# Performance work log

Measured on AMD Instinct MI355X. Metric: run time of the kernel, lower is better.

The kernel has to match this reference:

```python
import jax, jax.numpy as jnp
import numpy as np

B, C, H, W = 8, 512, 32, 32
NH = 8
DH = C // NH
HW = H * W
LN_EPS = 1e-5
NORM_EPS = 1e-12  # torch F.normalize eps


def setup_inputs() -> dict:
    key = jax.random.key(0)
    ks = jax.random.split(key, 8)
    s = 0.02
    return {
        "x": jax.random.normal(ks[0], (B, C, H, W), dtype=jnp.float32),
        "qkv_w": jax.random.normal(ks[1], (3 * C, C), dtype=jnp.float32) * s,
        "proj_w": jax.random.normal(ks[2], (C, C), dtype=jnp.float32) * s,
        "proj_b": jnp.zeros((C,), dtype=jnp.float32),
        "temperature": jnp.ones((NH, 1, 1), dtype=jnp.float32),
        "ln_g": jnp.ones((C,), dtype=jnp.float32),
        "ln_b": jnp.zeros((C,), dtype=jnp.float32),
        "pos_embed": jax.random.normal(ks[3], (1, HW, C), dtype=jnp.float32) * s,
        "dw_w": jax.random.normal(ks[4], (C, 1, 3, 3), dtype=jnp.float32) * s,
        "dw_b": jnp.zeros((C,), dtype=jnp.float32),
        "pw_w": jax.random.normal(ks[5], (C, C, 1, 1), dtype=jnp.float32) * s,
        "pw_b": jnp.zeros((C,), dtype=jnp.float32),
    }


def _l2norm_tokens(t):
    # normalize along token axis (dim=-2), like F.normalize(t, dim=-2)
    n = jnp.sqrt(jnp.sum(t * t, axis=-2, keepdims=True))
    return t / jnp.maximum(n, NORM_EPS)


def _layernorm(t, g, b):
    mu = jnp.mean(t, axis=-1, keepdims=True)
    var = jnp.mean((t - mu) ** 2, axis=-1, keepdims=True)
    return (t - mu) * jax.lax.rsqrt(var + LN_EPS) * g + b


def _dsconv(t, dw_w, dw_b, pw_w, pw_b):
    # depthwise 3x3 SAME + pointwise 1x1, NCHW / OIHW
    y = jax.lax.conv_general_dilated(
        t, dw_w, window_strides=(1, 1), padding="SAME",
        dimension_numbers=("NCHW", "OIHW", "NCHW"), feature_group_count=C)
    y = y + dw_b[None, :, None, None]
    y = jax.lax.conv_general_dilated(
        y, pw_w, window_strides=(1, 1), padding="SAME",
        dimension_numbers=("NCHW", "OIHW", "NCHW"))
    return y + pw_b[None, :, None, None]


def reference(x, qkv_w, proj_w, proj_b, temperature, ln_g, ln_b, pos_embed, dw_w, dw_b, pw_w, pw_b):
    save = x
    t = jnp.transpose(x.reshape(B, C, HW), (0, 2, 1))  # [B, HW, C]
    t = t + pos_embed
    # qkv projection (no bias)
    qkv = t @ qkv_w.T  # [B, HW, 3C]
    qkv = qkv.reshape(B, HW, 3, NH, DH).transpose(2, 0, 3, 1, 4)  # [3,B,NH,HW,DH]
    q, k, v = qkv[0], qkv[1], qkv[2]
    q = _l2norm_tokens(q)
    k = _l2norm_tokens(k)
    attn = jnp.einsum("bhnd,bhmd->bhnm", q, k) * temperature[None]  # [B,NH,HW,HW]
    attn = jax.nn.softmax(attn, axis=-1)
    o = jnp.einsum("bhnm,bhmd->bhnd", attn, v)  # [B,NH,HW,DH]
    o = o.transpose(0, 2, 1, 3).reshape(B, HW, C)
    o = o @ proj_w.T + proj_b
    o = _layernorm(o, ln_g, ln_b)
    o = jnp.transpose(o, (0, 2, 1)).reshape(B, C, H, W)
    o = o + save
    return o + _dsconv(o, dw_w, dw_b, pw_w, pw_b)
```

## Files before the change

kernel.cpp:

```cpp
#include <hip/hip_runtime.h>
#include <math.h>

#define BB_ 8
#define C_ 512
#define C3_ 1536
#define HW_ 1024
#define NH_ 8
#define DH_ 64
#define HH_ 32
#define WW_ 32

typedef __attribute__((ext_vector_type(8))) short short8;
typedef __attribute__((ext_vector_type(8))) unsigned short ushort8;
typedef __attribute__((ext_vector_type(4))) unsigned short ushort4_t;
typedef __attribute__((ext_vector_type(4))) float f32x4;
typedef unsigned short ushort;

__device__ inline ushort f2bf(float f) {
  union { float f; unsigned u; } v;
  v.f = f;
  unsigned r = v.u + 0x7fffu + ((v.u >> 16) & 1u);
  return (ushort)(r >> 16);
}
__device__ inline float bf2f(ushort u) {
  union { unsigned u; float f; } v;
  v.u = ((unsigned)u) << 16;
  return v.f;
}

#define GLD16(gptr, lptr)                                                     \
  __builtin_amdgcn_global_load_lds(                                           \
      (const __attribute__((address_space(1))) unsigned int*)(gptr),          \
      (__attribute__((address_space(3))) unsigned int*)(lptr), 16, 0, 0)

__global__ void cvt_weights_kernel(const float* __restrict__ qkv_w,
                                   const float* __restrict__ proj_w,
                                   const float* __restrict__ pw_w,
                                   ushort* __restrict__ dst) {
  int i = blockIdx.x * 256 + threadIdx.x;
  if (i < 786432) dst[i] = f2bf(qkv_w[i]);
  else if (i < 1048576) dst[i] = f2bf(proj_w[i - 786432]);
  else dst[i] = f2bf(pw_w[i - 1048576]);
}

__global__ __launch_bounds__(256) void add_pos_kernel(
    const float* __restrict__ x, const float* __restrict__ pos,
    ushort* __restrict__ t, ushort* __restrict__ xT) {
  __shared__ float tile[64][65];
  const int tid = threadIdx.x;
  const int n0 = blockIdx.x * 64, c0 = blockIdx.y * 64, b = blockIdx.z;
#pragma unroll
  for (int it = 0; it < 4; it++) {
    int c_l = (tid >> 4) + it * 16;
    int n_l4 = (tid & 15) * 4;
    float4 v = *(const float4*)&x[((size_t)(b * C_ + c0 + c_l)) * HW_ + n0 + n_l4];
    tile[c_l][n_l4 + 0] = v.x;
    tile[c_l][n_l4 + 1] = v.y;
    tile[c_l][n_l4 + 2] = v.z;
    tile[c_l][n_l4 + 3] = v.w;
  }
  __syncthreads();
#pragma unroll
  for (int it = 0; it < 4; it++) {
    int n_l = (tid >> 4) + it * 16;
    int c_l4 = (tid & 15) * 4;
    size_t token = (size_t)(b * HW_ + n0 + n_l);
    float4 pv = *(const float4*)&pos[(n0 + n_l) * C_ + c0 + c_l4];
    float xv0 = tile[c_l4 + 0][n_l], xv1 = tile[c_l4 + 1][n_l];
    float xv2 = tile[c_l4 + 2][n_l], xv3 = tile[c_l4 + 3][n_l];
    ushort4_t tb = {f2bf(xv0 + pv.x), f2bf(xv1 + pv.y), f2bf(xv2 + pv.z),
                    f2bf(xv3 + pv.w)};
    ushort4_t xb = {f2bf(xv0), f2bf(xv1), f2bf(xv2), f2bf(xv3)};
    *(ushort4_t*)&t[token * C_ + c0 + c_l4] = tb;
    *(ushort4_t*)&xT[token * C_ + c0 + c_l4] = xb;
  }
}

__global__ __launch_bounds__(256) void gemm_128(
    const ushort* __restrict__ A, const ushort* __restrict__ Wm,
    ushort* __restrict__ out, int N, int K) {
  __shared__ alignas(16) ushort As[128 * 32];
  __shared__ alignas(16) ushort Bs[128 * 32];
  const int bn = blockIdx.x * 128, bm = blockIdx.y * 128;
  const int tid = threadIdx.x;
  const int w = tid >> 6, lane = tid & 63;
  const int wm = 64 * (w & 1), wn = 64 * (w >> 1);
  const int l15 = lane & 15, lq = lane >> 4;

  f32x4 acc[4][4];
#pragma unroll
  for (int i = 0; i < 4; i++)
#pragma unroll
    for (int j = 0; j < 4; j++) acc[i][j] = (f32x4){0.f, 0.f, 0.f, 0.f};

  const int srr = lane >> 2, sq1 = lane & 3;

  for (int k0 = 0; k0 < K; k0 += 32) {
    __syncthreads();
#pragma unroll
    for (int j = 0; j < 2; j++) {
      int r = 32 * w + 16 * j + srr;
      int q = (sq1 - (r >> 1)) & 3;
      GLD16(A + (size_t)(bm + r) * K + k0 + q * 8, &As[(32 * w + 16 * j) * 32]);
      GLD16(Wm + (size_t)(bn + r) * K + k0 + q * 8, &Bs[(32 * w + 16 * j) * 32]);
    }
    __syncthreads();
    short8 af[4], bf[4];
#pragma unroll
    for (int nt = 0; nt < 4; nt++) {
      int r = wm + nt * 16 + l15;
      af[nt] = *(const short8*)&As[r * 32 + (((lq + (r >> 1)) & 3) * 8)];
      int c = wn + nt * 16 + l15;
      bf[nt] = *(const short8*)&Bs[c * 32 + (((lq + (c >> 1)) & 3) * 8)];
    }
#pragma unroll
    for (int i = 0; i < 4; i++)
#pragma unroll
      for (int j = 0; j < 4; j++)
        acc[i][j] = __builtin_amdgcn_mfma_f32_16x16x32_bf16(af[i], bf[j],
                                                            acc[i][j], 0, 0, 0);
  }

#pragma unroll
  for (int i = 0; i < 4; i++) {
#pragma unroll
    for (int j = 0; j < 4; j++) {
      int c = bn + wn + j * 16 + l15;
#pragma unroll
      for (int r = 0; r < 4; r++) {
        int m = bm + wm + i * 16 + lq * 4 + r;
        out[(size_t)m * N + c] = f2bf(acc[i][j][r]);
      }
    }
  }
}

template <int EPI>
__global__ __launch_bounds__(256) void gemm_n64(
    const ushort* __restrict__ A, const ushort* __restrict__ Wm,
    const float* __restrict__ bias, float* __restrict__ out,
    const float* __restrict__ resid, int N, int K) {
  __shared__ alignas(16) ushort As[128 * 32];
  __shared__ alignas(16) ushort Bs[64 * 32];
  const int bn = blockIdx.x * 64, bm = blockIdx.y * 128;
  const int tid = threadIdx.x;
  const int w = tid >> 6, lane = tid & 63;
  const int wm = 64 * (w & 1), wn = 32 * (w >> 1);
  const int l15 = lane & 15, lq = lane >> 4;

  f32x4 acc[4][2];
#pragma unroll
  for (int i = 0; i < 4; i++)
#pragma unroll
    for (int j = 0; j < 2; j++) acc[i][j] = (f32x4){0.f, 0.f, 0.f, 0.f};

  const int srr = lane >> 2, sq1 = lane & 3;

  for (int k0 = 0; k0 < K; k0 += 32) {
    __syncthreads();
#pragma unroll
    for (int j = 0; j < 2; j++) {
      int r = 32 * w + 16 * j + srr;
      int q = (sq1 - (r >> 1)) & 3;
      GLD16(A + (size_t)(bm + r) * K + k0 + q * 8, &As[(32 * w + 16 * j) * 32]);
    }
    {
      int r = 16 * w + srr;
      int q = (sq1 - (r >> 1)) & 3;
      GLD16(Wm + (size_t)(bn + r) * K + k0 + q * 8, &Bs[(16 * w) * 32]);
    }
    __syncthreads();
    short8 af[4], bf[2];
#pragma unroll
    for (int nt = 0; nt < 4; nt++) {
      int r = wm + nt * 16 + l15;
      af[nt] = *(const short8*)&As[r * 32 + (((lq + (r >> 1)) & 3) * 8)];
    }
#pragma unroll
    for (int j = 0; j < 2; j++) {
      int c = wn + j * 16 + l15;
      bf[j] = *(const short8*)&Bs[c * 32 + (((lq + (c >> 1)) & 3) * 8)];
    }
#pragma unroll
    for (int i = 0; i < 4; i++)
#pragma unroll
      for (int j = 0; j < 2; j++)
        acc[i][j] = __builtin_amdgcn_mfma_f32_16x16x32_bf16(af[i], bf[j],
                                                            acc[i][j], 0, 0, 0);
  }

#pragma unroll
  for (int i = 0; i < 4; i++) {
#pragma unroll
    for (int j = 0; j < 2; j++) {
      int c = bn + wn + j * 16 + l15;
      float bv = bias[c];
#pragma unroll
      for (int r = 0; r < 4; r++) {
        int m = bm + wm + i * 16 + lq * 4 + r;
        float v = acc[i][j][r] + bv;
        if (EPI == 1) {
          out[(size_t)m * N + c] = v;
        } else {
          int b = m >> 10, s = m & (HW_ - 1);
          out[((size_t)(b * C_ + c)) * HW_ + s] = v + resid[(size_t)m * C_ + c];
        }
      }
    }
  }
}

__global__ __launch_bounds__(256) void qk_norms_stage1(
    const ushort* __restrict__ qkv, float* __restrict__ partials) {
  __shared__ float smq[32][65], smk[32][65];
  const int blk = blockIdx.x;
  const int bh = blk >> 3, seg = blk & 7;
  const int b = bh >> 3, h = bh & 7;
  const int tid = threadIdx.x;
  const int trow = tid >> 3, chunk = tid & 7;
  float sq[8] = {}, sk[8] = {};
  const ushort* base = qkv + (size_t)b * HW_ * C3_ + h * 64 + chunk * 8;
#pragma unroll
  for (int i = 0; i < 4; i++) {
    int n = seg * 128 + i * 32 + trow;
    const ushort* p = base + (size_t)n * C3_;
    ushort8 q8 = *(const ushort8*)p;
    ushort8 k8 = *(const ushort8*)(p + C_);
#pragma unroll
    for (int j = 0; j < 8; j++) {
      float qv = bf2f(q8[j]), kv = bf2f(k8[j]);
      sq[j] += qv * qv;
      sk[j] += kv * kv;
    }
  }
#pragma unroll
  for (int j = 0; j < 8; j++) {
    smq[trow][chunk * 8 + j] = sq[j];
    smk[trow][chunk * 8 + j] = sk[j];
  }
  __syncthreads();
  if (tid < 64) {
    float s = 0.f;
    for (int i = 0; i < 32; i++) s += smq[i][tid];
    partials[((size_t)(bh * 8 + seg) * 2 + 0) * 64 + tid] = s;
  } else if (tid < 128) {
    int d = tid - 64;
    float s = 0.f;
    for (int i = 0; i < 32; i++) s += smk[i][d];
    partials[((size_t)(bh * 8 + seg) * 2 + 1) * 64 + d] = s;
  }
}

__global__ void qk_norms_stage2(const float* __restrict__ partials,
                                float* __restrict__ invq,
                                float* __restrict__ invk) {
  const int bh = blockIdx.x;
  const int tid = threadIdx.x;
  const int which = tid >> 6, d = tid & 63;
  float s = 0.f;
#pragma unroll
  for (int seg = 0; seg < 8; seg++)
    s += partials[((size_t)(bh * 8 + seg) * 2 + which) * 64 + d];
  float r = 1.0f / fmaxf(sqrtf(s), 1e-12f);
  if (which == 0) invq[bh * 64 + d] = r;
  else invk[bh * 64 + d] = r;
}

__global__ __launch_bounds__(512) void attn_mfma_kernel(
    const ushort* __restrict__ qkv, const float* __restrict__ invq,
    const float* __restrict__ invk, const float* __restrict__ temp,
    ushort* __restrict__ o) {
  __shared__ alignas(16) ushort Ks[64 * 64];
  __shared__ alignas(16) ushort Vts[64][88];
  __shared__ alignas(16) ushort Ps[8][16][88];

  const int tid = threadIdx.x;
  const int w = tid >> 6, lane = tid & 63;
  const int qgrp = lane >> 4, lcol = lane & 15;
  const int bh = blockIdx.x >> 3;
  const int qt = blockIdx.x & 7;
  const int b = bh >> 3, h = bh & 7;
  const int q0 = qt * 128;

  short8 qf[2];
  {
    const int m = q0 + w * 16 + lcol;
    const ushort* qrow = qkv + ((size_t)(b * HW_ + m)) * C3_ + h * 64;
    const float tmp = temp[h];
#pragma unroll
    for (int kc = 0; kc < 2; kc++) {
      union { short8 v; ushort u[8]; } pk;
#pragma unroll
      for (int j = 0; j < 8; j++) {
        int d = kc * 32 + qgrp * 8 + j;
        float s = invq[bh * 64 + d] * invk[bh * 64 + d] * tmp;
        pk.u[j] = f2bf(bf2f(qrow[d]) * s);
      }
      qf[kc] = pk.v;
    }
  }

  f32x4 of[4];
  float lsum[4] = {0.f, 0.f, 0.f, 0.f};
#pragma unroll
  for (int nt = 0; nt < 4; nt++) of[nt] = (f32x4){0.f, 0.f, 0.f, 0.f};

  const ushort* kg = qkv + (size_t)b * HW_ * C3_ + C_ + h * 64;

  const int srow = tid >> 3;
  const int sc = tid & 7;
  const int scg = sc ^ (srow & 7);
  const int vcol = (((srow >> 3) + sc) & 7) * 8 + (srow & 7);

  for (int kt = 0; kt < 16; kt++) {
    __syncthreads();
    GLD16(kg + (size_t)(kt * 64 + srow) * C3_ + scg * 8, &Ks[w * 512]);
    {
      const ushort* vsrc = kg + C_ + (size_t)(kt * 64 + srow) * C3_ + sc * 8;
      ushort8 vv = *(const ushort8*)vsrc;
#pragma unroll
      for (int j = 0; j < 8; j++) Vts[sc * 8 + j][vcol] = vv[j];
    }
    __syncthreads();

    f32x4 sfr[4];
#pragma unroll
    for (int nt = 0; nt < 4; nt++) sfr[nt] = (f32x4){0.f, 0.f, 0.f, 0.f};
#pragma unroll
    for (int kc = 0; kc < 2; kc++) {
#pragma unroll
      for (int nt = 0; nt < 4; nt++) {
        int row = nt * 16 + lcol;
        short8 kf = *(const short8*)
            &Ks[row * 64 + (((kc * 4 + qgrp) ^ (row & 7)) * 8)];
        sfr[nt] =
            __builtin_amdgcn_mfma_f32_16x16x32_bf16(qf[kc], kf, sfr[nt], 0, 0, 0);
      }
    }

#pragma unroll
    for (int nt = 0; nt < 4; nt++) {
#pragma unroll
      for (int r = 0; r < 4; r++) {
        float e = __expf(sfr[nt][r]);
        lsum[r] += e;
        Ps[w][qgrp * 4 + r][nt * 16 + lcol] = f2bf(e);
      }
    }

#pragma unroll
    for (int kc = 0; kc < 2; kc++) {
      short8 pf = *(const short8*)&Ps[w][lcol][kc * 32 + qgrp * 8];
#pragma unroll
      for (int nt = 0; nt < 4; nt++) {
        int d = nt * 16 + lcol;
        int cph = ((kc * 4 + qgrp) + (d >> 3)) & 7;
        short8 vf = *(const short8*)&Vts[d][cph * 8];
        of[nt] =
            __builtin_amdgcn_mfma_f32_16x16x32_bf16(pf, vf, of[nt], 0, 0, 0);
      }
    }
  }

  float inv[4];
#pragma unroll
  for (int r = 0; r < 4; r++) {
    float s = lsum[r];
    s += __shfl_xor(s, 1);
    s += __shfl_xor(s, 2);
    s += __shfl_xor(s, 4);
    s += __shfl_xor(s, 8);
    inv[r] = 1.0f / s;
  }
#pragma unroll
  for (int nt = 0; nt < 4; nt++) {
#pragma unroll
    for (int r = 0; r < 4; r++) {
      int m = q0 + w * 16 + qgrp * 4 + r;
      o[((size_t)(b * HW_ + m)) * C_ + h * 64 + nt * 16 + lcol] =
          f2bf(of[nt][r] * inv[r]);
    }
  }
}

__global__ void ln_residual_kernel(float* __restrict__ po, const ushort* xT,
                                   const float* __restrict__ g,
                                   const float* __restrict__ bb, ushort* ybf) {
  int token = blockIdx.x;
  int t = threadIdx.x;
  float* row = po + (size_t)token * C_;
  float v0 = row[t], v1 = row[t + 256];
  float s = v0 + v1;
#pragma unroll
  for (int off = 32; off; off >>= 1) s += __shfl_xor(s, off);
  __shared__ float wr[4];
  if ((t & 63) == 0) wr[t >> 6] = s;
  __syncthreads();
  float mu = (wr[0] + wr[1] + wr[2] + wr[3]) * (1.0f / C_);
  float d0 = v0 - mu, d1 = v1 - mu;
  float vs = d0 * d0 + d1 * d1;
#pragma unroll
  for (int off = 32; off; off >>= 1) vs += __shfl_xor(vs, off);
  __syncthreads();
  if ((t & 63) == 0) wr[t >> 6] = vs;
  __syncthreads();
  float var = (wr[0] + wr[1] + wr[2] + wr[3]) * (1.0f / C_);
  float rstd = rsqrtf(var + 1e-5f);
  float r0 = bf2f(xT[(size_t)token * C_ + t]);
  float r1 = bf2f(xT[(size_t)token * C_ + t + 256]);
  float o0 = d0 * rstd * g[t] + bb[t] + r0;
  float o1 = d1 * rstd * g[t + 256] + bb[t + 256] + r1;
  row[t] = o0;
  row[t + 256] = o1;
  ybf[(size_t)token * C_ + t] = f2bf(o0);
  ybf[(size_t)token * C_ + t + 256] = f2bf(o1);
}

__global__ __launch_bounds__(256) void dwconv_kernel(
    const ushort* __restrict__ y, const float* __restrict__ w,
    const float* __restrict__ bias, ushort* __restrict__ out) {
  const int cg = threadIdx.x & 63, tg = threadIdx.x >> 6;
  const int c0 = cg * 8;
  float wreg[9][8], breg[8];
#pragma unroll
  for (int j = 0; j < 8; j++) {
    breg[j] = bias[c0 + j];
#pragma unroll
    for (int kk = 0; kk < 9; kk++) wreg[kk][j] = w[(c0 + j) * 9 + kk];
  }
  for (int i = 0; i < 4; i++) {
    int token = blockIdx.x * 16 + tg * 4 + i;
    int b = token >> 10, s = token & (HW_ - 1);
    int hh = s >> 5, ww = s & 31;
    float acc[8];
#pragma unroll
    for (int j = 0; j < 8; j++) acc[j] = breg[j];
#pragma unroll
    for (int ky = 0; ky < 3; ky++) {
      int yy = hh + ky - 1;
      if (yy < 0 || yy >= HH_) continue;
#pragma unroll
      for (int kx = 0; kx < 3; kx++) {
        int xx = ww + kx - 1;
        if (xx < 0 || xx >= WW_) continue;
        ushort8 v8 = *(const ushort8*)
            &y[((size_t)(b * HW_ + yy * 32 + xx)) * C_ + c0];
        const float* wk = wreg[ky * 3 + kx];
#pragma unroll
        for (int j = 0; j < 8; j++) acc[j] += wk[j] * bf2f(v8[j]);
      }
    }
    ushort8 pk;
#pragma unroll
    for (int j = 0; j < 8; j++) pk[j] = f2bf(acc[j]);
    *(ushort8*)&out[(size_t)token * C_ + c0] = pk;
  }
}

extern "C" void kernel_launch(void* const* d_in, const int* in_sizes, int n_in,
                              void* d_out, int out_size, void* d_ws,
                              size_t ws_size, hipStream_t stream) {
  const float* x = (const float*)d_in[0];
  const float* qkv_w = (const float*)d_in[1];
  const float* proj_w = (const float*)d_in[2];
  const float* proj_b = (const float*)d_in[3];
  const float* temperature = (const float*)d_in[4];
  const float* ln_g = (const float*)d_in[5];
  const float* ln_b = (const float*)d_in[6];
  const float* pos = (const float*)d_in[7];
  const float* dw_w = (const float*)d_in[8];
  const float* dw_b = (const float*)d_in[9];
  const float* pw_w = (const float*)d_in[10];
  const float* pw_b = (const float*)d_in[11];
  float* out = (float*)d_out;

  float* ws = (float*)d_ws;
  ushort* qkv_bf = (ushort*)ws;
  ushort* t_bf = (ushort*)(ws + (size_t)6 * 1024 * 1024);
  float* proj_out = ws + (size_t)8 * 1024 * 1024;
  ushort* xT_bf = (ushort*)(ws + (size_t)12 * 1024 * 1024);
  ushort* wts = (ushort*)(ws + (size_t)14 * 1024 * 1024);
  ushort* qkvw_bf = wts;
  ushort* projw_bf = wts + 786432;
  ushort* pww_bf = wts + 1048576;
  float* invq = ws + (size_t)15 * 1024 * 1024;
  float* invk = invq + 512;
  float* partials = invk + 512;

  const int M = BB_ * HW_;

  cvt_weights_kernel<<<1310720 / 256, 256, 0, stream>>>(qkv_w, proj_w, pw_w,
                                                        wts);
  add_pos_kernel<<<dim3(16, 8, 8), 256, 0, stream>>>(x, pos, t_bf, xT_bf);
  gemm_128<<<dim3(C3_ / 128, M / 128), 256, 0, stream>>>(t_bf, qkvw_bf,
                                                         qkv_bf, C3_, C_);
  qk_norms_stage1<<<512, 256, 0, stream>>>(qkv_bf, partials);
  qk_norms_stage2<<<64, 128, 0, stream>>>(partials, invq, invk);
  attn_mfma_kernel<<<BB_ * NH_ * (HW_ / 128), 512, 0, stream>>>(
      qkv_bf, invq, invk, temperature, t_bf);
  gemm_n64<1><<<dim3(C_ / 64, M / 128), 256, 0, stream>>>(
      t_bf, projw_bf, proj_b, proj_out, nullptr, C_, C_);
  ln_residual_kernel<<<M, 256, 0, stream>>>(proj_out, xT_bf, ln_g, ln_b,
                                            xT_bf);
  dwconv_kernel<<<M / 16, 256, 0, stream>>>(xT_bf, dw_w, dw_b, t_bf);
  gemm_n64<2><<<dim3(C_ / 64, M / 128), 256, 0, stream>>>(
      t_bf, pww_bf, pw_b, out, proj_out, C_, C_);
}
```

Baseline: 218.5 us.

## Pre-transpose V and keep P in registers via transposed-score MFMA

Adds a separate kernel that writes V transposed per head to workspace, so the attention kernel can load V tiles into LDS with async global-to-LDS copies instead of doing per-element scattered LDS stores. The QK^T MFMA operands are swapped so that the exponentiated scores come out in the layout a 16x16x16 bf16 MFMA needs as its B operand. P therefore stays in registers and the LDS round trip through the Ps buffer goes away. The cost is an extra kernel launch plus an extra read and write of V, and smaller-K MFMAs for the PV product.

```diff
diff --git a/kernel.cpp b/kernel.cpp
--- a/kernel.cpp
+++ b/kernel.cpp
@@ -11,6 +11,7 @@
 #define WW_ 32
 
 typedef __attribute__((ext_vector_type(8))) short short8;
+typedef __attribute__((ext_vector_type(4))) short short4v;
 typedef __attribute__((ext_vector_type(8))) unsigned short ushort8;
 typedef __attribute__((ext_vector_type(4))) unsigned short ushort4_t;
 typedef __attribute__((ext_vector_type(4))) float f32x4;
@@ -32,6 +33,21 @@
   __builtin_amdgcn_global_load_lds(                                           \
       (const __attribute__((address_space(1))) unsigned int*)(gptr),          \
       (__attribute__((address_space(3))) unsigned int*)(lptr), 16, 0, 0)
+
+__device__ inline f32x4 pv_mfma(const ushort* vp, short4v pf, f32x4 acc) {
+#if __has_builtin(__builtin_amdgcn_mfma_f32_16x16x16_bf16)
+  short4v vf = *(const short4v*)vp;
+  return __builtin_amdgcn_mfma_f32_16x16x16_bf16(vf, pf, acc, 0, 0, 0);
+#elif __has_builtin(__builtin_amdgcn_mfma_f32_16x16x16bf16_1k)
+  short4v vf = *(const short4v*)vp;
+  return __builtin_amdgcn_mfma_f32_16x16x16bf16_1k(vf, pf, acc, 0, 0, 0);
+#else
+  short4v v4 = *(const short4v*)vp;
+  short8 vf = {v4[0], v4[1], v4[2], v4[3], 0, 0, 0, 0};
+  short8 pf8 = {pf[0], pf[1], pf[2], pf[3], 0, 0, 0, 0};
+  return __builtin_amdgcn_mfma_f32_16x16x32_bf16(vf, pf8, acc, 0, 0, 0);
+#endif
+}
 
 __global__ void cvt_weights_kernel(const float* __restrict__ qkv_w,
                                    const float* __restrict__ proj_w,
@@ -210,6 +226,35 @@
   }
 }
 
+__global__ __launch_bounds__(256) void vt_kernel(const ushort* __restrict__ qkv,
+                                                 ushort* __restrict__ vt) {
+  __shared__ ushort tileT[64][72];
+  const int bh = blockIdx.x >> 2, seg = blockIdx.x & 3;
+  const int b = bh >> 3, h = bh & 7;
+  const int tid = threadIdx.x;
+  const ushort* src = qkv + (size_t)b * HW_ * C3_ + 2 * C_ + h * 64;
+  for (int t = 0; t < 4; t++) {
+    int n0 = seg * 256 + t * 64;
+    __syncthreads();
+#pragma unroll
+    for (int it = 0; it < 2; it++) {
+      int row = it * 32 + (tid >> 3);
+      int c8 = (tid & 7) * 8;
+      ushort8 v = *(const ushort8*)&src[(size_t)(n0 + row) * C3_ + c8];
+#pragma unroll
+      for (int j = 0; j < 8; j++) tileT[c8 + j][row] = v[j];
+    }
+    __syncthreads();
+#pragma unroll
+    for (int it = 0; it < 2; it++) {
+      int d = it * 32 + (tid >> 3);
+      int nch = (tid & 7) * 8;
+      ushort8 o8 = *(const ushort8*)&tileT[d][nch];
+      *(ushort8*)&vt[((size_t)(bh * 64 + d)) * HW_ + n0 + nch] = o8;
+    }
+  }
+}
+
 __global__ __launch_bounds__(256) void qk_norms_stage1(
     const ushort* __restrict__ qkv, float* __restrict__ partials) {
   __shared__ float smq[32][65], smk[32][65];
@@ -267,16 +312,15 @@
 }
 
 __global__ __launch_bounds__(512) void attn_mfma_kernel(
-    const ushort* __restrict__ qkv, const float* __restrict__ invq,
-    const float* __restrict__ invk, const float* __restrict__ temp,
-    ushort* __restrict__ o) {
+    const ushort* __restrict__ qkv, const ushort* __restrict__ vt,
+    const float* __restrict__ invq, const float* __restrict__ invk,
+    const float* __restrict__ temp, ushort* __restrict__ o) {
   __shared__ alignas(16) ushort Ks[64 * 64];
-  __shared__ alignas(16) ushort Vts[64][88];
-  __shared__ alignas(16) ushort Ps[8][16][88];
+  __shared__ alignas(16) ushort Vts[64 * 64];
 
   const int tid = threadIdx.x;
   const int w = tid >> 6, lane = tid & 63;
-  const int qgrp = lane >> 4, lcol = lane & 15;
+  const int quad = lane >> 4, lcol = lane & 15;
   const int bh = blockIdx.x >> 3;
   const int qt = blockIdx.x & 7;
   const int b = bh >> 3, h = bh & 7;
@@ -292,7 +336,7 @@
       union { short8 v; ushort u[8]; } pk;
 #pragma unroll
       for (int j = 0; j < 8; j++) {
-        int d = kc * 32 + qgrp * 8 + j;
+        int d = kc * 32 + quad * 8 + j;
         float s = invq[bh * 64 + d] * invk[bh * 64 + d] * tmp;
         pk.u[j] = f2bf(bf2f(qrow[d]) * s);
       }
@@ -300,27 +344,22 @@
     }
   }
 
-  f32x4 of[4];
-  float lsum[4] = {0.f, 0.f, 0.f, 0.f};
-#pragma unroll
-  for (int nt = 0; nt < 4; nt++) of[nt] = (f32x4){0.f, 0.f, 0.f, 0.f};
+  f32x4 ot[4];
+#pragma unroll
+  for (int dt = 0; dt < 4; dt++) ot[dt] = (f32x4){0.f, 0.f, 0.f, 0.f};
+  float lsum = 0.f;
 
   const ushort* kg = qkv + (size_t)b * HW_ * C3_ + C_ + h * 64;
+  const ushort* vg = vt + (size_t)(bh * 64) * HW_;
 
   const int srow = tid >> 3;
   const int sc = tid & 7;
   const int scg = sc ^ (srow & 7);
-  const int vcol = (((srow >> 3) + sc) & 7) * 8 + (srow & 7);
 
   for (int kt = 0; kt < 16; kt++) {
     __syncthreads();
     GLD16(kg + (size_t)(kt * 64 + srow) * C3_ + scg * 8, &Ks[w * 512]);
-    {
-      const ushort* vsrc = kg + C_ + (size_t)(kt * 64 + srow) * C3_ + sc * 8;
-      ushort8 vv = *(const ushort8*)vsrc;
-#pragma unroll
-      for (int j = 0; j < 8; j++) Vts[sc * 8 + j][vcol] = vv[j];
-    }
+    GLD16(vg + (size_t)srow * HW_ + kt * 64 + scg * 8, &Vts[w * 512]);
     __syncthreads();
 
     f32x4 sfr[4];
@@ -332,54 +371,49 @@
       for (int nt = 0; nt < 4; nt++) {
         int row = nt * 16 + lcol;
         short8 kf = *(const short8*)
-            &Ks[row * 64 + (((kc * 4 + qgrp) ^ (row & 7)) * 8)];
+            &Ks[row * 64 + (((kc * 4 + quad) ^ (row & 7)) * 8)];
         sfr[nt] =
-            __builtin_amdgcn_mfma_f32_16x16x32_bf16(qf[kc], kf, sfr[nt], 0, 0, 0);
-      }
-    }
-
+            __builtin_amdgcn_mfma_f32_16x16x32_bf16(kf, qf[kc], sfr[nt], 0, 0, 0);
+      }
+    }
+
+    ushort pk[4][4];
 #pragma unroll
     for (int nt = 0; nt < 4; nt++) {
 #pragma unroll
       for (int r = 0; r < 4; r++) {
         float e = __expf(sfr[nt][r]);
-        lsum[r] += e;
-        Ps[w][qgrp * 4 + r][nt * 16 + lcol] = f2bf(e);
-      }
-    }
-
-#pragma unroll
-    for (int kc = 0; kc < 2; kc++) {
-      short8 pf = *(const short8*)&Ps[w][lcol][kc * 32 + qgrp * 8];
-#pragma unroll
-      for (int nt = 0; nt < 4; nt++) {
-        int d = nt * 16 + lcol;
-        int cph = ((kc * 4 + qgrp) + (d >> 3)) & 7;
-        short8 vf = *(const short8*)&Vts[d][cph * 8];
-        of[nt] =
-            __builtin_amdgcn_mfma_f32_16x16x32_bf16(pf, vf, of[nt], 0, 0, 0);
-      }
-    }
-  }
-
-  float inv[4];
-#pragma unroll
-  for (int r = 0; r < 4; r++) {
-    float s = lsum[r];
-    s += __shfl_xor(s, 1);
-    s += __shfl_xor(s, 2);
-    s += __shfl_xor(s, 4);
-    s += __shfl_xor(s, 8);
-    inv[r] = 1.0f / s;
-  }
-#pragma unroll
-  for (int nt = 0; nt < 4; nt++) {
-#pragma unroll
-    for (int r = 0; r < 4; r++) {
-      int m = q0 + w * 16 + qgrp * 4 + r;
-      o[((size_t)(b * HW_ + m)) * C_ + h * 64 + nt * 16 + lcol] =
-          f2bf(of[nt][r] * inv[r]);
-    }
+        lsum += e;
+        pk[nt][r] = f2bf(e);
+      }
+    }
+
+#pragma unroll
+    for (int nt = 0; nt < 4; nt++) {
+      short4v pf = {(short)pk[nt][0], (short)pk[nt][1], (short)pk[nt][2],
+                    (short)pk[nt][3]};
+      int key = nt * 16 + quad * 4;
+#pragma unroll
+      for (int dt = 0; dt < 4; dt++) {
+        int d = dt * 16 + lcol;
+        const ushort* vp =
+            &Vts[d * 64 + (((key >> 3) ^ (d & 7)) * 8) + (key & 7)];
+        ot[dt] = pv_mfma(vp, pf, ot[dt]);
+      }
+    }
+  }
+
+  lsum += __shfl_xor(lsum, 16);
+  lsum += __shfl_xor(lsum, 32);
+  const float inv = 1.0f / lsum;
+
+  const int m = q0 + w * 16 + lcol;
+  ushort* orow = o + ((size_t)(b * HW_ + m)) * C_ + h * 64;
+#pragma unroll
+  for (int dt = 0; dt < 4; dt++) {
+    ushort4_t pkb = {f2bf(ot[dt][0] * inv), f2bf(ot[dt][1] * inv),
+                     f2bf(ot[dt][2] * inv), f2bf(ot[dt][3] * inv)};
+    *(ushort4_t*)&orow[dt * 16 + quad * 4] = pkb;
   }
 }
 
@@ -486,6 +520,7 @@
   float* invq = ws + (size_t)15 * 1024 * 1024;
   float* invk = invq + 512;
   float* partials = invk + 512;
+  ushort* vtb = (ushort*)(ws + (size_t)16 * 1024 * 1024);
 
   const int M = BB_ * HW_;
 
@@ -494,10 +529,11 @@
   add_pos_kernel<<<dim3(16, 8, 8), 256, 0, stream>>>(x, pos, t_bf, xT_bf);
   gemm_128<<<dim3(C3_ / 128, M / 128), 256, 0, stream>>>(t_bf, qkvw_bf,
                                                          qkv_bf, C3_, C_);
+  vt_kernel<<<256, 256, 0, stream>>>(qkv_bf, vtb);
   qk_norms_stage1<<<512, 256, 0, stream>>>(qkv_bf, partials);
   qk_norms_stage2<<<64, 128, 0, stream>>>(partials, invq, invk);
   attn_mfma_kernel<<<BB_ * NH_ * (HW_ / 128), 512, 0, stream>>>(
-      qkv_bf, invq, invk, temperature, t_bf);
+      qkv_bf, vtb, invq, invk, temperature, t_bf);
   gemm_n64<1><<<dim3(C_ / 64, M / 128), 256, 0, stream>>>(
       t_bf, projw_bf, proj_b, proj_out, nullptr, C_, C_);
   ln_residual_kernel<<<M, 256, 0, stream>>>(proj_out, xT_bf, ln_g, ln_b,
```

After: 220.8 us. About the same (+1.0%).
